# Kernel tuning notes

Measured on AMD Instinct MI355X. Metric: run time of the kernel, lower is better.

## Reference

```python
import jax, jax.numpy as jnp
import numpy as np

N_NODES = 20000
N_EDGES = 100000
NODE_IN = 4
EDGE_IN = 4
HIDDEN = 64
N_GRAPHS = 64
LN_EPS = 1e-5


def _glorot(key, shape):
    fan_in, fan_out = shape[0], shape[1]
    lim = jnp.sqrt(6.0 / (fan_in + fan_out))
    return jax.random.uniform(key, shape, jnp.float32, -lim, lim)


def setup_inputs() -> dict:
    key = jax.random.key(0)
    ks = jax.random.split(key, 24)
    inp = {
        "x": jax.random.normal(ks[0], (N_NODES, NODE_IN), jnp.float32),
        "edge_index": jax.random.randint(ks[1], (2, N_EDGES), 0, N_NODES),
        "edge_attr": jax.random.normal(ks[2], (N_EDGES, EDGE_IN), jnp.float32),
        "batch": jnp.sort(jax.random.randint(ks[3], (N_NODES,), 0, N_GRAPHS)),
        # layer 1: edge MLP edge_in->64->node_in*hidden, root lin, bias, LN
        "eW1_1": _glorot(ks[4], (EDGE_IN, 64)),
        "eb1_1": jnp.zeros((64,), jnp.float32),
        "eW2_1": _glorot(ks[5], (64, NODE_IN * HIDDEN)),
        "eb2_1": jnp.zeros((NODE_IN * HIDDEN,), jnp.float32),
        "root1": _glorot(ks[6], (NODE_IN, HIDDEN)),
        "bias1": jnp.zeros((HIDDEN,), jnp.float32),
        "g1": jnp.ones((HIDDEN,), jnp.float32),
        "b1": jnp.zeros((HIDDEN,), jnp.float32),
        # layer 2: edge MLP edge_in->128->hidden*hidden, root lin, bias, LN
        "eW1_2": _glorot(ks[7], (EDGE_IN, 128)),
        "eb1_2": jnp.zeros((128,), jnp.float32),
        "eW2_2": _glorot(ks[8], (128, HIDDEN * HIDDEN)),
        "eb2_2": jnp.zeros((HIDDEN * HIDDEN,), jnp.float32),
        "root2": _glorot(ks[9], (HIDDEN, HIDDEN)),
        "bias2": jnp.zeros((HIDDEN,), jnp.float32),
        "g2": jnp.ones((HIDDEN,), jnp.float32),
        "b2": jnpp_zeros if False else jnp.zeros((HIDDEN,), jnp.float32),
    }
    return inp


def _nnconv(h, src, dst, edge_attr, eW1, eb1, eW2, eb2, root, bias, in_ch, out_ch):
    # per-edge weight matrix from edge MLP: [E, in_ch, out_ch]
    ew = jnp.maximum(edge_attr @ eW1 + eb1, 0.0) @ eW2 + eb2
    ew = ew.reshape(-1, in_ch, out_ch)
    # gather src features, per-edge small matmul
    msg = jnp.einsum("ei,eio->eo", h[src], ew)  # [E, out_ch]
    # scatter-mean to dst
    agg = jax.ops.segment_sum(msg, dst, num_segments=N_NODES)
    deg = jax.ops.segment_sum(jnp.ones((msg.shape[0],), msg.dtype), dst, num_segments=N_NODES)
    agg = agg / jnp.maximum(deg, 1.0)[:, None]
    return agg + h @ root + bias


def _layernorm(v, g, b):
    mu = jnp.mean(v, axis=-1, keepdims=True)
    var = jnp.mean((v - mu) ** 2, axis=-1, keepdims=True)
    return (v - mu) * jax.lax.rsqrt(var + LN_EPS) * g + b


def reference(x, edge_index, edge_attr, batch,
              eW1_1, eb1_1, eW2_1, eb2_1, root1, bias1, g1, b1,
              eW1_2, eb1_2, eW2_2, eb2_2, root2, bias2, g2, b2):
    src, dst = edge_index[0], edge_index[1]
    h = _nnconv(x, src, dst, edge_attr, eW1_1, eb1_1, eW2_1, eb2_1, root1, bias1, NODE_IN, HIDDEN)
    h = _layernorm(jnp.maximum(h, 0.0), g1, b1)  # dropout is identity in eval
    h = _nnconv(h, src, dst, edge_attr, eW1_2, eb1_2, eW2_2, eb2_2, root2, bias2, HIDDEN, HIDDEN)
    h = _layernorm(jnp.maximum(h, 0.0), g2, b2)
    # global mean pool over graphs
    num = jax.ops.segment_sum(h, batch, num_segments=N_GRAPHS)
    cnt = jax.ops.segment_sum(jnp.ones((h.shape[0],), h.dtype), batch, num_segments=N_GRAPHS)
    return num / jnp.maximum(cnt, 1.0)[:, None]
```

## Files before the change

### kernel.cpp

```cpp
#include <hip/hip_runtime.h>
#include <hip/hip_bf16.h>
#include <hip/hip_fp16.h>

#define NN 20000
#define NE 100000
#define NGR 64

using bf16 = __hip_bfloat16;
typedef __attribute__((ext_vector_type(8))) short v8s;
typedef __attribute__((ext_vector_type(4))) float v4f;
typedef _Float16 h2f __attribute__((ext_vector_type(2)));

__device__ __forceinline__ float ldf(const void* p, int idx, int isbf) {
  if (isbf) return __bfloat162float(((const bf16*)p)[idx]);
  return ((const float*)p)[idx];
}
__device__ __forceinline__ unsigned short f2bfbits(float v) {
  unsigned int b = __float_as_uint(v);
  b += 0x7fffu + ((b >> 16) & 1u);
  return (unsigned short)(b >> 16);
}

__device__ __forceinline__ unsigned int pkh2(float a, float b) {
#if __has_builtin(__builtin_amdgcn_cvt_pkrtz)
  auto r = __builtin_amdgcn_cvt_pkrtz(a, b);
  return __builtin_bit_cast(unsigned int, r);
#else
  unsigned int lo = __half_as_ushort(__float2half(a));
  unsigned int hi = __half_as_ushort(__float2half(b));
  return lo | (hi << 16);
#endif
}
__device__ __forceinline__ float dot2a(unsigned int z, unsigned int q, float c) {
#if __has_builtin(__builtin_amdgcn_fdot2)
  return __builtin_amdgcn_fdot2(__builtin_bit_cast(h2f, z),
                                __builtin_bit_cast(h2f, q), c, false);
#else
  h2f zh = __builtin_bit_cast(h2f, z), qh = __builtin_bit_cast(h2f, q);
  return c + (float)zh.x * (float)qh.x + (float)zh.y * (float)qh.y;
#endif
}

__global__ __launch_bounds__(64) void k_detect(const unsigned short* __restrict__ xr,
                                               int* __restrict__ flag) {
  const int t = threadIdx.x;
  int cnt = 0;
#pragma unroll
  for (int j = 0; j < 4; j++) {
    unsigned short w = xr[t * 4 + j];
    int ex = (w >> 7) & 0xFF;
    cnt += (ex >= 118 && ex <= 131) ? 1 : 0;
  }
#pragma unroll
  for (int m = 32; m >= 1; m >>= 1) cnt += __shfl_xor(cnt, m, 64);
  if (t == 0) *flag = (cnt >= 192) ? 1 : 0;
}

__global__ __launch_bounds__(256) void k_deg(const int* __restrict__ ei,
                                             int* __restrict__ deg_src,
                                             int* __restrict__ deg_in) {
  int e = blockIdx.x * 256 + threadIdx.x;
  if (e < NE) {
    atomicAdd(&deg_src[ei[e]], 1);
    atomicAdd(&deg_in[ei[NE + e]], 1);
  }
}

__global__ __launch_bounds__(256) void k_scan(const int* __restrict__ deg,
                                              int* __restrict__ off,
                                              int* __restrict__ cur) {
  constexpr int T = 256, CH = 80;
  __shared__ int sums[T];
  const int t = threadIdx.x;
  const int base = t * CH;
  int s = 0;
  for (int j = 0; j < CH; j++) {
    int i = base + j;
    s += (i < NN) ? deg[i] : 0;
  }
  sums[t] = s;
  __syncthreads();
  for (int st = 1; st < T; st <<= 1) {
    int v = (t >= st) ? sums[t - st] : 0;
    __syncthreads();
    sums[t] += v;
    __syncthreads();
  }
  int run = sums[t] - s;
  for (int j = 0; j < CH; j++) {
    int i = base + j;
    if (i < NN) {
      int v = deg[i];
      off[i] = run;
      cur[i] = run;
      run += v;
    }
  }
  if (t == T - 1) off[NN] = sums[T - 1];
}

__global__ __launch_bounds__(256) void k_scatter(const int* __restrict__ ei,
                                                 int* __restrict__ cur,
                                                 int* __restrict__ ebs) {
  int e = blockIdx.x * 256 + threadIdx.x;
  if (e < NE) {
    int p = atomicAdd(&cur[ei[e]], 1);
    if (p >= 0 && p < NE) ebs[p] = e;
  }
}

template <int KH, int IN>
__global__ __launch_bounds__(256) void k_shuffle(const void* __restrict__ W2,
                                                 unsigned short* __restrict__ W2s,
                                                 const int* __restrict__ flag) {
  const int f = *flag;
  int t = blockIdx.x * 256 + threadIdx.x;
  int lane = t & 63, F = t >> 6;
  int ks = F & 1, ot = (F >> 1) & 3, k2 = F >> 3;
  int quad = lane >> 4, col = lane & 15;
  unsigned short tmp[8];
#pragma unroll
  for (int j = 0; j < 8; j++) {
    int i = ks * 32 + quad * 8 + j;
    tmp[j] = f2bfbits(ldf(W2, k2 * (IN * 64) + i * 64 + ot * 16 + col, f));
  }
  *(uint4*)(W2s + (size_t)F * 512 + lane * 8) = *(uint4*)tmp;
}

template <int IN, int KH, int HMODE, int QMFMA>
__global__ __launch_bounds__(512, 4) void k_fused2(
    const void* __restrict__ h_in, const void* __restrict__ eW1,
    const void* __restrict__ eb1, const void* __restrict__ W2,
    const unsigned short* __restrict__ W2s, const void* __restrict__ eb2,
    const void* __restrict__ ea, const int* __restrict__ ei,
    const int* __restrict__ src_off, const int* __restrict__ ebs,
    float* __restrict__ agg, const int* __restrict__ flag) {
  constexpr int NPG = 16, KC = 16, NCH = KH / KC, EB = 128;
  constexpr int QNS = (KC / 2) * 64 + 4;
  constexpr int ZROW = 10;

  __shared__ float hA[NPG][IN];
  __shared__ float r2[NPG][64];
  __shared__ __align__(16) unsigned int Qc[NPG * QNS];
  __shared__ float eW1S[4][KH];
  __shared__ float ebS[KH];
  __shared__ float eaS[EB][4];
  __shared__ __align__(16) unsigned int zB[EB * ZROW];
  __shared__ int esrcS[EB], edstS[EB];
  __shared__ __align__(16) unsigned short hF[QMFMA ? 2 : 1][64][8];

  const int f = *flag;
  const int tid = threadIdx.x;
  const int o = tid & 63;
  const int kq = tid >> 6;
  const int n0 = blockIdx.x * NPG;

  for (int idx = tid; idx < NPG * IN; idx += 512) {
    int n = idx / IN, i = idx - n * IN;
    hA[n][i] = (HMODE == 1) ? ((const float*)h_in)[(n0 + n) * IN + i]
                            : ldf(h_in, (n0 + n) * IN + i, f);
  }
  for (int idx = tid; idx < 4 * KH; idx += 512)
    ((float*)eW1S)[idx] = ldf(eW1, idx, f);
  for (int idx = tid; idx < KH; idx += 512) ebS[idx] = ldf(eb1, idx, f);
  __syncthreads();

  {
    const int nb = kq * 2;
    float a0 = 0.f, a1 = 0.f;
    for (int i = 0; i < IN; i++) {
      float wv = ldf(eb2, i * 64 + o, f);
      a0 += hA[nb + 0][i] * wv;
      a1 += hA[nb + 1][i] * wv;
    }
    r2[nb + 0][o] = a0;
    r2[nb + 1][o] = a1;
  }
  if constexpr (QMFMA) {
    if (tid < 128) {
      int l = tid & 63, ks = tid >> 6;
#pragma unroll
      for (int j = 0; j < 8; j++)
        hF[ks][l][j] = f2bfbits(hA[l & 15][ks * 32 + (l >> 4) * 8 + j]);
    }
  }
  __syncthreads();

  v8s aF0 = {}, aF1 = {};
  if constexpr (QMFMA) {
    aF0 = *(const v8s*)&hF[0][o][0];
    aF1 = *(const v8s*)&hF[1][o][0];
  }

  const int estart = src_off[n0];
  const int ecount = src_off[n0 + NPG] - estart;

  for (int b = 0; b < ecount; b += EB) {
    const int bc = min(EB, ecount - b);
    __syncthreads();
    if (tid < bc) {
      int eid = ebs[estart + b + tid];
      esrcS[tid] = ei[eid] - n0;
      edstS[tid] = ei[NE + eid];
#pragma unroll
      for (int i = 0; i < 4; i++) eaS[tid][i] = ldf(ea, eid * 4 + i, f);
    }
    __syncthreads();

    float msg[EB / 8];
#pragma unroll
    for (int j = 0; j < EB / 8; j++) msg[j] = 0.f;
    const int lo = (bc * kq) >> 3, hi = (bc * (kq + 1)) >> 3;

    for (int c = 0; c < NCH; c++) {
      v4f acc8[8];
      float accv[NPG * 2];
      if constexpr (QMFMA) {
#pragma unroll
        for (int nt = 0; nt < 8; nt++) {
          acc8[nt] = (v4f){0.f, 0.f, 0.f, 0.f};
          const int k2 = c * KC + kq * 2 + (nt >> 2);
          const int Fb = (k2 * 4 + (nt & 3)) * 2;
          v8s b0 = *(const v8s*)(W2s + (size_t)Fb * 512 + o * 8);
          v8s b1 = *(const v8s*)(W2s + (size_t)(Fb + 1) * 512 + o * 8);
          acc8[nt] =
              __builtin_amdgcn_mfma_f32_16x16x32_bf16(aF0, b0, acc8[nt], 0, 0, 0);
          acc8[nt] =
              __builtin_amdgcn_mfma_f32_16x16x32_bf16(aF1, b1, acc8[nt], 0, 0, 0);
        }
      } else {
        const int kg0 = c * KC + kq * 2;
        const int w2base = kg0 * (IN * 64) + o;
        float w0[IN], w1[IN];
#pragma unroll
        for (int j = 0; j < IN; j++) {
          w0[j] = ldf(W2, w2base + j * 64, f);
          w1[j] = ldf(W2, w2base + IN * 64 + j * 64, f);
        }
#pragma unroll
        for (int n = 0; n < NPG; n++) {
          float a0 = 0.f, a1 = 0.f;
#pragma unroll
          for (int j = 0; j < IN; j++) {
            float hv = hA[n][j];
            a0 += hv * w0[j];
            a1 += hv * w1[j];
          }
          accv[n * 2 + 0] = a0;
          accv[n * 2 + 1] = a1;
        }
      }
      const int ze = tid & 127, kseg = tid >> 7;
      float zv[4];
      if (ze < bc) {
#pragma unroll
        for (int jj = 0; jj < 4; jj++) {
          int k2 = c * KC + kseg * 4 + jj;
          float a = ebS[k2];
#pragma unroll
          for (int i = 0; i < 4; i++) a += eaS[ze][i] * eW1S[i][k2];
          zv[jj] = fmaxf(a, 0.f);
        }
      }
      __syncthreads();
      if constexpr (QMFMA) {
        const int quad = o >> 4;
#pragma unroll
        for (int nt = 0; nt < 4; nt++) {
          const int o2 = nt * 16 + (o & 15);
#pragma unroll
          for (int r = 0; r < 4; r++)
            Qc[(quad * 4 + r) * QNS + kq * 64 + o2] =
                pkh2(acc8[nt][r], acc8[nt + 4][r]);
        }
      } else {
#pragma unroll
        for (int n = 0; n < NPG; n++)
          Qc[n * QNS + kq * 64 + o] = pkh2(accv[n * 2 + 0], accv[n * 2 + 1]);
      }
      if (ze < bc) {
        uint2 p;
        p.x = pkh2(zv[0], zv[1]);
        p.y = pkh2(zv[2], zv[3]);
        *(uint2*)&zB[ze * ZROW + kseg * 2] = p;
      }
      __syncthreads();
      unsigned int q0 = 0, q1 = 0, q2 = 0, q3 = 0, q4 = 0, q5 = 0, q6 = 0,
                   q7 = 0;
      int sprev = -1;
#pragma unroll
      for (int j = 0; j < EB / 8; j++) {
        const int e = lo + j;
        if (e < hi) {
          const int s = esrcS[e];
          if (s != sprev) {
            const unsigned int* qp = &Qc[s * QNS + o];
            q0 = qp[0 * 64]; q1 = qp[1 * 64]; q2 = qp[2 * 64]; q3 = qp[3 * 64];
            q4 = qp[4 * 64]; q5 = qp[5 * 64]; q6 = qp[6 * 64]; q7 = qp[7 * 64];
            sprev = s;
          }
          const uint2 za = *(const uint2*)&zB[e * ZROW + 0];
          const uint2 zb = *(const uint2*)&zB[e * ZROW + 2];
          const uint2 zc = *(const uint2*)&zB[e * ZROW + 4];
          const uint2 zd = *(const uint2*)&zB[e * ZROW + 6];
          float m = msg[j];
          m = dot2a(za.x, q0, m);
          m = dot2a(za.y, q1, m);
          m = dot2a(zb.x, q2, m);
          m = dot2a(zb.y, q3, m);
          m = dot2a(zc.x, q4, m);
          m = dot2a(zc.y, q5, m);
          m = dot2a(zd.x, q6, m);
          m = dot2a(zd.y, q7, m);
          msg[j] = m;
        }
      }
    }
#pragma unroll
    for (int j = 0; j < EB / 8; j++) {
      const int e = lo + j;
      if (e < hi)
        atomicAdd(&agg[(size_t)edstS[e] * 64 + o], msg[j] + r2[esrcS[e]][o]);
    }
  }
}

__device__ __forceinline__ float wave_sum(float v) {
#pragma unroll
  for (int m = 32; m >= 1; m >>= 1) v += __shfl_xor(v, m, 64);
  return v;
}

__global__ __launch_bounds__(256, 4) void k_node1(
    const float* __restrict__ agg1, const int* __restrict__ deg_in,
    const void* __restrict__ x, const void* __restrict__ root1,
    const void* __restrict__ bias1, const void* __restrict__ g1,
    const void* __restrict__ b1, float* __restrict__ h1,
    const int* __restrict__ flag) {
  constexpr int NPW = 8;
  const int f = *flag;
  const int tid = threadIdx.x;
  const int o = tid & 63;
  const int w = tid >> 6;
  float r1c[4];
#pragma unroll
  for (int i = 0; i < 4; i++) r1c[i] = ldf(root1, i * 64 + o, f);
  const float bs = ldf(bias1, o, f);
  const float gv = ldf(g1, o, f);
  const float bv = ldf(b1, o, f);
  const int wid = blockIdx.x * 4 + w;
  const int nbeg = wid * NPW;
  const int nend = min(nbeg + NPW, NN);
  for (int n = nbeg; n < nend; n++) {
    float v = agg1[(size_t)n * 64 + o] / fmaxf((float)deg_in[n], 1.f) + bs;
#pragma unroll
    for (int i = 0; i < 4; i++) v += ldf(x, n * 4 + i, f) * r1c[i];
    v = fmaxf(v, 0.f);
    const float mu = wave_sum(v) * (1.f / 64.f);
    const float d = v - mu;
    const float var = wave_sum(d * d) * (1.f / 64.f);
    h1[(size_t)n * 64 + o] = d * rsqrtf(var + 1e-5f) * gv + bv;
  }
}

__global__ __launch_bounds__(256, 4) void k_node2(
    const float* __restrict__ agg2, const int* __restrict__ deg_in,
    const float* __restrict__ h1, const void* __restrict__ root2,
    const void* __restrict__ bias2, const void* __restrict__ g2,
    const void* __restrict__ b2, const int* __restrict__ batch,
    float* __restrict__ psum, float* __restrict__ pcnt,
    const int* __restrict__ flag) {
  constexpr int NPW = 8;
  __shared__ float hS[4][64];
  const int f = *flag;
  const int tid = threadIdx.x;
  const int o = tid & 63;
  const int w = tid >> 6;
  float r2c[64];
#pragma unroll
  for (int i = 0; i < 64; i++) r2c[i] = ldf(root2, i * 64 + o, f);
  const float bs = ldf(bias2, o, f);
  const float gv = ldf(g2, o, f);
  const float bv = ldf(b2, o, f);
  const int wid = blockIdx.x * 4 + w;
  const int nbeg = wid * NPW;
  const int nend = min(nbeg + NPW, NN);
  float acc = 0.f;
  int curbi = -1, cnt = 0;
  for (int n = nbeg; n < nend; n++) {
    hS[w][o] = h1[(size_t)n * 64 + o];
    float v = agg2[(size_t)n * 64 + o] / fmaxf((float)deg_in[n], 1.f) + bs;
#pragma unroll
    for (int i = 0; i < 64; i++) v += hS[w][i] * r2c[i];
    v = fmaxf(v, 0.f);
    const float mu = wave_sum(v) * (1.f / 64.f);
    const float d = v - mu;
    const float var = wave_sum(d * d) * (1.f / 64.f);
    const float out = d * rsqrtf(var + 1e-5f) * gv + bv;
    const int bi = batch[n];
    if (bi != curbi) {
      if (curbi >= 0) {
        atomicAdd(&psum[curbi * 64 + o], acc);
        if (o == 0) atomicAdd(&pcnt[curbi], (float)cnt);
      }
      acc = 0.f;
      cnt = 0;
      curbi = bi;
    }
    acc += out;
    cnt++;
  }
  if (curbi >= 0) {
    atomicAdd(&psum[curbi * 64 + o], acc);
    if (o == 0) atomicAdd(&pcnt[curbi], (float)cnt);
  }
}

__global__ __launch_bounds__(256) void k_out(const float* __restrict__ psum,
                                             const float* __restrict__ pcnt,
                                             void* __restrict__ out,
                                             const int* __restrict__ flag) {
  const int idx = blockIdx.x * 256 + threadIdx.x;
  float v = psum[idx] / fmaxf(pcnt[idx >> 6], 1.f);
  if (*flag)
    ((bf16*)out)[idx] = __float2bfloat16(v);
  else
    ((float*)out)[idx] = v;
}

extern "C" void kernel_launch(void* const* d_in, const int* in_sizes, int n_in,
                              void* d_out, int out_size, void* d_ws,
                              size_t ws_size, hipStream_t stream) {
  (void)in_sizes; (void)n_in; (void)out_size; (void)ws_size;
  const void* x = d_in[0];
  const int* ei = (const int*)d_in[1];
  const void* ea = d_in[2];
  const int* batch = (const int*)d_in[3];
  const void* eW1_1 = d_in[4];
  const void* eb1_1 = d_in[5];
  const void* eW2_1 = d_in[6];
  const void* eb2_1 = d_in[7];
  const void* root1 = d_in[8];
  const void* bias1 = d_in[9];
  const void* g1 = d_in[10];
  const void* b1 = d_in[11];
  const void* eW1_2 = d_in[12];
  const void* eb1_2 = d_in[13];
  const void* eW2_2 = d_in[14];
  const void* eb2_2 = d_in[15];
  const void* root2 = d_in[16];
  const void* bias2 = d_in[17];
  const void* g2 = d_in[18];
  const void* b2 = d_in[19];

  char* w = (char*)d_ws;
  size_t off = 0;
  auto alloc = [&](size_t bytes) -> void* {
    void* p = w + off;
    off = (off + bytes + 255) & ~(size_t)255;
    return p;
  };
  float* agg1 = (float*)alloc((size_t)NN * 64 * 4);
  float* agg2 = (float*)alloc((size_t)NN * 64 * 4);
  float* psum = (float*)alloc((size_t)NGR * 64 * 4);
  float* pcnt = (float*)alloc((size_t)NGR * 4);
  int* deg_src = (int*)alloc((size_t)NN * 4);
  int* deg_in = (int*)alloc((size_t)NN * 4);
  const size_t zero_bytes = off;
  int* src_off = (int*)alloc((size_t)(NN + 1) * 4);
  int* cur = (int*)alloc((size_t)NN * 4);
  int* ebs = (int*)alloc((size_t)NE * 4);
  int* flag = (int*)alloc(256);
  float* h1 = (float*)alloc((size_t)NN * 64 * 4);
  unsigned short* W2s = (unsigned short*)alloc((size_t)128 * 8 * 64 * 8 * 2);

  hipMemsetAsync(d_ws, 0, zero_bytes, stream);

  k_detect<<<1, 64, 0, stream>>>((const unsigned short*)x, flag);
  k_deg<<<(NE + 255) / 256, 256, 0, stream>>>(ei, deg_src, deg_in);
  k_scan<<<1, 256, 0, stream>>>(deg_src, src_off, cur);
  k_scatter<<<(NE + 255) / 256, 256, 0, stream>>>(ei, cur, ebs);
  k_shuffle<128, 64><<<256, 256, 0, stream>>>(eW2_2, W2s, flag);
  k_fused2<4, 64, 0, 0><<<NN / 16, 512, 0, stream>>>(
      x, eW1_1, eb1_1, eW2_1, W2s, eb2_1, ea, ei, src_off, ebs, agg1, flag);
  k_node1<<<(NN + 8 * 4 - 1) / (8 * 4), 256, 0, stream>>>(
      agg1, deg_in, x, root1, bias1, g1, b1, h1, flag);
  k_fused2<64, 128, 1, 1><<<NN / 16, 512, 0, stream>>>(
      h1, eW1_2, eb1_2, eW2_2, W2s, eb2_2, ea, ei, src_off, ebs, agg2, flag);
  k_node2<<<(NN + 8 * 4 - 1) / (8 * 4), 256, 0, stream>>>(
      agg2, deg_in, h1, root2, bias2, g2, b2, batch, psum, pcnt, flag);
  k_out<<<(NGR * 64) / 256, 256, 0, stream>>>(psum, pcnt, d_out, flag);
}
```

Measured before the change: 411.3 us.

## Split hidden-dimension chunks of the edge-MLP contraction across a second grid dimension

The loop over KC-sized hidden chunks inside each fused NNConv block is moved onto blockIdx.y, so each block handles one chunk for its 16 source nodes. Each block then does one Q computation and one z pass, and issues its own atomicAdd of partial messages, with the bias term r2 added only by chunk 0. This gives more parallelism and smaller per-block shared memory and register state. The cost is more global atomics (one per chunk per edge per output) and redundant edge-metadata loads in every chunk block. Padding constants (QNS, ZROW) also change.

```diff
diff --git a/kernel.cpp b/kernel.cpp
--- a/kernel.cpp
+++ b/kernel.cpp
@@ -135,15 +135,15 @@
     const void* __restrict__ ea, const int* __restrict__ ei,
     const int* __restrict__ src_off, const int* __restrict__ ebs,
     float* __restrict__ agg, const int* __restrict__ flag) {
-  constexpr int NPG = 16, KC = 16, NCH = KH / KC, EB = 128;
-  constexpr int QNS = (KC / 2) * 64 + 4;
-  constexpr int ZROW = 10;
+  constexpr int NPG = 16, KC = 16, EB = 128;
+  constexpr int QNS = (KC / 2) * 64 + 1;
+  constexpr int ZROW = 8;
 
   __shared__ float hA[NPG][IN];
   __shared__ float r2[NPG][64];
   __shared__ __align__(16) unsigned int Qc[NPG * QNS];
-  __shared__ float eW1S[4][KH];
-  __shared__ float ebS[KH];
+  __shared__ float eW1S[4][KC];
+  __shared__ float ebS[KC];
   __shared__ float eaS[EB][4];
   __shared__ __align__(16) unsigned int zB[EB * ZROW];
   __shared__ int esrcS[EB], edstS[EB];
@@ -153,6 +153,7 @@
   const int tid = threadIdx.x;
   const int o = tid & 63;
   const int kq = tid >> 6;
+  const int c = blockIdx.y;
   const int n0 = blockIdx.x * NPG;
 
   for (int idx = tid; idx < NPG * IN; idx += 512) {
@@ -160,12 +161,14 @@
     hA[n][i] = (HMODE == 1) ? ((const float*)h_in)[(n0 + n) * IN + i]
                             : ldf(h_in, (n0 + n) * IN + i, f);
   }
-  for (int idx = tid; idx < 4 * KH; idx += 512)
-    ((float*)eW1S)[idx] = ldf(eW1, idx, f);
-  for (int idx = tid; idx < KH; idx += 512) ebS[idx] = ldf(eb1, idx, f);
+  if (tid < 4 * KC) {
+    int i = tid / KC, kk = tid - i * KC;
+    eW1S[i][kk] = ldf(eW1, i * KH + c * KC + kk, f);
+  }
+  if (tid < KC) ebS[tid] = ldf(eb1, c * KC + tid, f);
   __syncthreads();
 
-  {
+  if (c == 0) {
     const int nb = kq * 2;
     float a0 = 0.f, a1 = 0.f;
     for (int i = 0; i < IN; i++) {
@@ -186,10 +189,51 @@
   }
   __syncthreads();
 
-  v8s aF0 = {}, aF1 = {};
   if constexpr (QMFMA) {
-    aF0 = *(const v8s*)&hF[0][o][0];
-    aF1 = *(const v8s*)&hF[1][o][0];
+    v8s aF0 = *(const v8s*)&hF[0][o][0];
+    v8s aF1 = *(const v8s*)&hF[1][o][0];
+    v4f acc8[8];
+#pragma unroll
+    for (int nt = 0; nt < 8; nt++) {
+      acc8[nt] = (v4f){0.f, 0.f, 0.f, 0.f};
+      const int k2 = c * KC + kq * 2 + (nt >> 2);
+      const int Fb = (k2 * 4 + (nt & 3)) * 2;
+      v8s b0 = *(const v8s*)(W2s + (size_t)Fb * 512 + o * 8);
+      v8s b1 = *(const v8s*)(W2s + (size_t)(Fb + 1) * 512 + o * 8);
+      acc8[nt] =
+          __builtin_amdgcn_mfma_f32_16x16x32_bf16(aF0, b0, acc8[nt], 0, 0, 0);
+      acc8[nt] =
+          __builtin_amdgcn_mfma_f32_16x16x32_bf16(aF1, b1, acc8[nt], 0, 0, 0);
+    }
+    const int quad = o >> 4;
+#pragma unroll
+    for (int nt = 0; nt < 4; nt++) {
+      const int o2 = nt * 16 + (o & 15);
+#pragma unroll
+      for (int r = 0; r < 4; r++)
+        Qc[(quad * 4 + r) * QNS + kq * 64 + o2] =
+            pkh2(acc8[nt][r], acc8[nt + 4][r]);
+    }
+  } else {
+    const int kg0 = c * KC + kq * 2;
+    const int w2base = kg0 * (IN * 64) + o;
+    float w0[IN], w1[IN];
+#pragma unroll
+    for (int j = 0; j < IN; j++) {
+      w0[j] = ldf(W2, w2base + j * 64, f);
+      w1[j] = ldf(W2, w2base + IN * 64 + j * 64, f);
+    }
+#pragma unroll
+    for (int n = 0; n < NPG; n++) {
+      float a0 = 0.f, a1 = 0.f;
+#pragma unroll
+      for (int j = 0; j < IN; j++) {
+        float hv = hA[n][j];
+        a0 += hv * w0[j];
+        a1 += hv * w1[j];
+      }
+      Qc[n * QNS + kq * 64 + o] = pkh2(a0, a1);
+    }
   }
 
   const int estart = src_off[n0];
@@ -207,120 +251,55 @@
     }
     __syncthreads();
 
-    float msg[EB / 8];
-#pragma unroll
-    for (int j = 0; j < EB / 8; j++) msg[j] = 0.f;
+    const int ze = tid & 127, kseg = tid >> 7;
+    if (ze < bc) {
+      float zv[4];
+#pragma unroll
+      for (int jj = 0; jj < 4; jj++) {
+        int kk = kseg * 4 + jj;
+        float a = ebS[kk];
+#pragma unroll
+        for (int i = 0; i < 4; i++) a += eaS[ze][i] * eW1S[i][kk];
+        zv[jj] = fmaxf(a, 0.f);
+      }
+      uint2 p;
+      p.x = pkh2(zv[0], zv[1]);
+      p.y = pkh2(zv[2], zv[3]);
+      *(uint2*)&zB[ze * ZROW + kseg * 2] = p;
+    }
+    __syncthreads();
+
     const int lo = (bc * kq) >> 3, hi = (bc * (kq + 1)) >> 3;
-
-    for (int c = 0; c < NCH; c++) {
-      v4f acc8[8];
-      float accv[NPG * 2];
-      if constexpr (QMFMA) {
-#pragma unroll
-        for (int nt = 0; nt < 8; nt++) {
-          acc8[nt] = (v4f){0.f, 0.f, 0.f, 0.f};
-          const int k2 = c * KC + kq * 2 + (nt >> 2);
-          const int Fb = (k2 * 4 + (nt & 3)) * 2;
-          v8s b0 = *(const v8s*)(W2s + (size_t)Fb * 512 + o * 8);
-          v8s b1 = *(const v8s*)(W2s + (size_t)(Fb + 1) * 512 + o * 8);
-          acc8[nt] =
-              __builtin_amdgcn_mfma_f32_16x16x32_bf16(aF0, b0, acc8[nt], 0, 0, 0);
-          acc8[nt] =
-              __builtin_amdgcn_mfma_f32_16x16x32_bf16(aF1, b1, acc8[nt], 0, 0, 0);
-        }
-      } else {
-        const int kg0 = c * KC + kq * 2;
-        const int w2base = kg0 * (IN * 64) + o;
-        float w0[IN], w1[IN];
-#pragma unroll
-        for (int j = 0; j < IN; j++) {
-          w0[j] = ldf(W2, w2base + j * 64, f);
-          w1[j] = ldf(W2, w2base + IN * 64 + j * 64, f);
-        }
-#pragma unroll
-        for (int n = 0; n < NPG; n++) {
-          float a0 = 0.f, a1 = 0.f;
-#pragma unroll
-          for (int j = 0; j < IN; j++) {
-            float hv = hA[n][j];
-            a0 += hv * w0[j];
-            a1 += hv * w1[j];
-          }
-          accv[n * 2 + 0] = a0;
-          accv[n * 2 + 1] = a1;
-        }
-      }
-      const int ze = tid & 127, kseg = tid >> 7;
-      float zv[4];
-      if (ze < bc) {
-#pragma unroll
-        for (int jj = 0; jj < 4; jj++) {
-          int k2 = c * KC + kseg * 4 + jj;
-          float a = ebS[k2];
-#pragma unroll
-          for (int i = 0; i < 4; i++) a += eaS[ze][i] * eW1S[i][k2];
-          zv[jj] = fmaxf(a, 0.f);
-        }
-      }
-      __syncthreads();
-      if constexpr (QMFMA) {
-        const int quad = o >> 4;
-#pragma unroll
-        for (int nt = 0; nt < 4; nt++) {
-          const int o2 = nt * 16 + (o & 15);
-#pragma unroll
-          for (int r = 0; r < 4; r++)
-            Qc[(quad * 4 + r) * QNS + kq * 64 + o2] =
-                pkh2(acc8[nt][r], acc8[nt + 4][r]);
-        }
-      } else {
-#pragma unroll
-        for (int n = 0; n < NPG; n++)
-          Qc[n * QNS + kq * 64 + o] = pkh2(accv[n * 2 + 0], accv[n * 2 + 1]);
-      }
-      if (ze < bc) {
-        uint2 p;
-        p.x = pkh2(zv[0], zv[1]);
-        p.y = pkh2(zv[2], zv[3]);
-        *(uint2*)&zB[ze * ZROW + kseg * 2] = p;
-      }
-      __syncthreads();
-      unsigned int q0 = 0, q1 = 0, q2 = 0, q3 = 0, q4 = 0, q5 = 0, q6 = 0,
-                   q7 = 0;
-      int sprev = -1;
-#pragma unroll
-      for (int j = 0; j < EB / 8; j++) {
-        const int e = lo + j;
-        if (e < hi) {
-          const int s = esrcS[e];
-          if (s != sprev) {
-            const unsigned int* qp = &Qc[s * QNS + o];
-            q0 = qp[0 * 64]; q1 = qp[1 * 64]; q2 = qp[2 * 64]; q3 = qp[3 * 64];
-            q4 = qp[4 * 64]; q5 = qp[5 * 64]; q6 = qp[6 * 64]; q7 = qp[7 * 64];
-            sprev = s;
-          }
-          const uint2 za = *(const uint2*)&zB[e * ZROW + 0];
-          const uint2 zb = *(const uint2*)&zB[e * ZROW + 2];
-          const uint2 zc = *(const uint2*)&zB[e * ZROW + 4];
-          const uint2 zd = *(const uint2*)&zB[e * ZROW + 6];
-          float m = msg[j];
-          m = dot2a(za.x, q0, m);
-          m = dot2a(za.y, q1, m);
-          m = dot2a(zb.x, q2, m);
-          m = dot2a(zb.y, q3, m);
-          m = dot2a(zc.x, q4, m);
-          m = dot2a(zc.y, q5, m);
-          m = dot2a(zd.x, q6, m);
-          m = dot2a(zd.y, q7, m);
-          msg[j] = m;
-        }
-      }
-    }
+    unsigned int q0 = 0, q1 = 0, q2 = 0, q3 = 0, q4 = 0, q5 = 0, q6 = 0,
+                 q7 = 0;
+    int sprev = -1;
 #pragma unroll
     for (int j = 0; j < EB / 8; j++) {
       const int e = lo + j;
-      if (e < hi)
-        atomicAdd(&agg[(size_t)edstS[e] * 64 + o], msg[j] + r2[esrcS[e]][o]);
+      if (e < hi) {
+        const int s = esrcS[e];
+        if (s != sprev) {
+          const unsigned int* qp = &Qc[s * QNS + o];
+          q0 = qp[0 * 64]; q1 = qp[1 * 64]; q2 = qp[2 * 64]; q3 = qp[3 * 64];
+          q4 = qp[4 * 64]; q5 = qp[5 * 64]; q6 = qp[6 * 64]; q7 = qp[7 * 64];
+          sprev = s;
+        }
+        const uint2 za = *(const uint2*)&zB[e * ZROW + 0];
+        const uint2 zb = *(const uint2*)&zB[e * ZROW + 2];
+        const uint2 zc = *(const uint2*)&zB[e * ZROW + 4];
+        const uint2 zd = *(const uint2*)&zB[e * ZROW + 6];
+        float m = 0.f;
+        m = dot2a(za.x, q0, m);
+        m = dot2a(za.y, q1, m);
+        m = dot2a(zb.x, q2, m);
+        m = dot2a(zb.y, q3, m);
+        m = dot2a(zc.x, q4, m);
+        m = dot2a(zc.y, q5, m);
+        m = dot2a(zd.x, q6, m);
+        m = dot2a(zd.y, q7, m);
+        if (c == 0) m += r2[s][o];
+        atomicAdd(&agg[(size_t)edstS[e] * 64 + o], m);
+      }
     }
   }
 }
@@ -481,11 +460,11 @@
   k_scan<<<1, 256, 0, stream>>>(deg_src, src_off, cur);
   k_scatter<<<(NE + 255) / 256, 256, 0, stream>>>(ei, cur, ebs);
   k_shuffle<128, 64><<<256, 256, 0, stream>>>(eW2_2, W2s, flag);
-  k_fused2<4, 64, 0, 0><<<NN / 16, 512, 0, stream>>>(
+  k_fused2<4, 64, 0, 0><<<dim3(NN / 16, 64 / 16), 512, 0, stream>>>(
       x, eW1_1, eb1_1, eW2_1, W2s, eb2_1, ea, ei, src_off, ebs, agg1, flag);
   k_node1<<<(NN + 8 * 4 - 1) / (8 * 4), 256, 0, stream>>>(
       agg1, deg_in, x, root1, bias1, g1, b1, h1, flag);
-  k_fused2<64, 128, 1, 1><<<NN / 16, 512, 0, stream>>>(
+  k_fused2<64, 128, 1, 1><<<dim3(NN / 16, 128 / 16), 512, 0, stream>>>(
       h1, eW1_2, eb1_2, eW2_2, W2s, eb2_2, ea, ei, src_off, ebs, agg2, flag);
   k_node2<<<(NN + 8 * 4 - 1) / (8 * 4), 256, 0, stream>>>(
       agg2, deg_in, h1, root2, bias2, g2, b2, batch, psum, pcnt, flag);
```

After: 491.5 us. +19.5%, slower.
